# Optimization experiments

Measured on AMD Instinct MI355X. Metric: run time of the kernel, lower is better.

Reference implementation:

```python
import jax, jax.numpy as jnp
import numpy as np

ALPHA = 0.001
TAU = 1.0
KAPPA = 1.0
N_ITER = 1


def setup_inputs() -> dict:
    key = jax.random.key(0)
    k1, k2, k3, k4, k5 = jax.random.split(key, 5)
    B, H, N, K = 8, 8, 512, 16
    mu = jax.random.normal(k1, (B, N, K), dtype=jnp.float32)
    # beta: softmax-like attention weights over j (positive, rows sum to 1)
    beta = jax.nn.softmax(jax.random.normal(k2, (B, H, N, N), dtype=jnp.float32), axis=-1)
    mu_prior = jax.random.normal(k3, (B, N, K), dtype=jnp.float32)
    phi = 0.1 * jax.random.normal(k4, (B, N, 3), dtype=jnp.float32)
    g = jax.random.normal(k5, (3, K, K), dtype=jnp.float32)
    generators = 0.5 * (g - jnp.swapaxes(g, -1, -2))  # skew-symmetric so(3) rep -> stable expm
    lr = jnp.asarray(0.05, dtype=jnp.float32)
    return {"mu": mu, "beta": beta, "mu_prior": mu_prior, "phi": phi,
            "generators": generators, "lr": lr}


def _transport(mu, phi, generators):
    # phi_algebra[b,n] = sum_g phi[b,n,g] * G_g  -> (B,N,K,K)
    B, N, K = mu.shape
    phi_alg = jnp.einsum('bng,gkl->bnkl', phi, generators)
    expm = jax.vmap(jax.scipy.linalg.expm)
    Om_i = expm(phi_alg.reshape(B * N, K, K)).reshape(B, N, K, K)
    Om_j_inv = expm((-phi_alg).reshape(B * N, K, K)).reshape(B, N, K, K)
    # mu_t[b,i,j] = Om_i[b,i] @ (Om_j_inv[b,j] @ mu[b,j])  (factored, avoids (B,N,N,K,K))
    v = jnp.einsum('bjlm,bjm->bjl', Om_j_inv, mu)          # (B,N,K)
    mu_t = jnp.einsum('bikl,bjl->bijk', Om_i, v)           # (B,N,N,K)
    return mu_t


def reference(mu, beta, mu_prior, phi, generators, lr):
    beta_avg = beta.mean(axis=1)                           # (B,N,N)
    mu_cur = mu
    for _ in range(N_ITER):
        grad_prior = ALPHA * (mu_cur - mu_prior)
        mu_t = _transport(mu_cur, phi, generators)         # (B,N,N,K)
        delta = mu_cur[:, :, None, :] - mu_t               # (B,N,N,K)
        # TERM 1: sum_j (beta_ij/tau) * delta_ij
        grad1 = jnp.einsum('bij,bijk->bik', beta_avg, delta) / TAU
        # TERM 2 (second-order): sum_j sum_k (beta_ij/kappa)(delta_jk - beta_ik) KL_ij gkl_ik
        #   = (1/kappa)[ sum_j beta_ij KL_ij gkl_ij - (sum_j beta_ij KL_ij) * sum_k beta_ik gkl_ik ]
        kl = jnp.sum(delta * delta, axis=-1) / (2.0 * TAU)  # (B,N,N)
        gkl = delta / TAU                                   # (B,N,N,K)
        w = beta_avg * kl                                   # (B,N,N)
        term1 = jnp.einsum('bij,bijk->bik', w, gkl)
        s = jnp.sum(w, axis=-1)                             # (B,N)
        bsum = jnp.einsum('bij,bijk->bik', beta_avg, gkl)
        grad2 = (term1 - s[..., None] * bsum) / KAPPA
        mu_cur = mu_cur - lr * (grad_prior + grad1 + grad2)
    return mu_cur
```

## Files before the change

### kernel.cpp

```cpp
#include <hip/hip_runtime.h>
#include <hip/hip_bf16.h>
#include <cstddef>
#include <cstdint>

#define B_ 8
#define H_ 8
#define N_ 512
#define K_ 16
#define NN_ (N_*N_)

static constexpr float ALPHA_C = 0.001f;

typedef float f32x4 __attribute__((ext_vector_type(4)));

#define LDSTRIDE 20

__device__ __forceinline__ void mm_rowB(const float* a, const float* Bbuf,
                                        int c0, f32x4& acc)
{
    #pragma unroll
    for (int k = 0; k < 16; ++k) {
        const f32x4 bk = *(const f32x4*)&Bbuf[k * LDSTRIDE + c0];
        acc.x = fmaf(a[k], bk.x, acc.x);
        acc.y = fmaf(a[k], bk.y, acc.y);
        acc.z = fmaf(a[k], bk.z, acc.z);
        acc.w = fmaf(a[k], bk.w, acc.w);
    }
}

__device__ __forceinline__ void read_row(const float* buf, int r, float* a)
{
    #pragma unroll
    for (int i = 0; i < 4; ++i) {
        const f32x4 t = *(const f32x4*)&buf[r * LDSTRIDE + 4 * i];
        a[4*i]   = t.x; a[4*i+1] = t.y; a[4*i+2] = t.z; a[4*i+3] = t.w;
    }
}

__device__ __forceinline__ void write_strip(float* buf, int r, int c0, f32x4 s)
{
    *(f32x4*)&buf[r * LDSTRIDE + c0] = s;
}

__global__ __launch_bounds__(256) void expm_beta_kernel(
    const float* __restrict__ mu, const float* __restrict__ phi,
    const float* __restrict__ gen, const float* __restrict__ beta,
    float* __restrict__ Om, float* __restrict__ v, float* __restrict__ q,
    float* __restrict__ bavg)
{
    __shared__ float lds[4][2][16 * LDSTRIDE];

    const int tid  = threadIdx.x;
    const int w    = tid >> 6, lane = tid & 63;
    const int r    = lane >> 2, c0 = (lane & 3) << 2;
    const int bn   = (blockIdx.x << 2) | w;
    const int bb   = bn >> 9;
    const int nn   = bn & 511;

    float* U0 = lds[w][0];
    float* U1 = lds[w][1];

    const float p0 = phi[bn*3+0], p1 = phi[bn*3+1], p2 = phi[bn*3+2];
    const int gidx = r * 16 + c0;
    const f32x4 g0 = *(const f32x4*)&gen[gidx];
    const f32x4 g1 = *(const f32x4*)&gen[256 + gidx];
    const f32x4 g2 = *(const f32x4*)&gen[512 + gidx];
    const float mur = mu[bn * 16 + r];

    const size_t betaBase = (((size_t)bb * H_) * N_ + nn) * N_;
    const float* bp = beta + betaBase + (lane << 2);
    f32x4 bt[16];
    #pragma unroll
    for (int h = 0; h < H_; ++h) {
        bt[2*h+0] = __builtin_nontemporal_load((const f32x4*)(bp + (size_t)h * NN_));
        bt[2*h+1] = __builtin_nontemporal_load((const f32x4*)(bp + (size_t)h * NN_ + 256));
    }

    f32x4 As;
    As.x = p0*g0.x + p1*g1.x + p2*g2.x;
    As.y = p0*g0.y + p1*g1.y + p2*g2.y;
    As.z = p0*g0.z + p1*g1.z + p2*g2.z;
    As.w = p0*g0.w + p1*g1.w + p2*g2.w;

    float t = As.x*As.x + As.y*As.y + As.z*As.z + As.w*As.w;
    #pragma unroll
    for (int m = 1; m <= 32; m <<= 1) t += __shfl_xor(t, m, 64);
    float theta = sqrtf(t);
    int s = 0;
    while (theta > 2.0f && s < 30) { theta *= 0.5f; ++s; }
    const float sc = exp2f((float)(-s));
    const f32x4 Xs = As * sc;

    write_strip(U0, r, c0, Xs);
    float xrow[16];
    read_row(U0, r, xrow);

    {
        const f32x4 rv0 = (((bt[0]+bt[2]) + (bt[4]+bt[6]))
                         + ((bt[8]+bt[10]) + (bt[12]+bt[14]))) * 0.125f;
        const f32x4 rv1 = (((bt[1]+bt[3]) + (bt[5]+bt[7]))
                         + ((bt[9]+bt[11]) + (bt[13]+bt[15]))) * 0.125f;
        float* bo = bavg + (size_t)bn * N_ + (lane << 2);
        *(f32x4*)bo         = rv0;
        *(f32x4*)(bo + 256) = rv1;
    }

    f32x4 a2s = {0.f, 0.f, 0.f, 0.f};
    mm_rowB(xrow, U0, c0, a2s);
    write_strip(U1, r, c0, a2s);

    f32x4 a3s = {0.f, 0.f, 0.f, 0.f};
    mm_rowB(xrow, U1, c0, a3s);

    float a2row[16];
    read_row(U1, r, a2row);
    f32x4 a4s = {0.f, 0.f, 0.f, 0.f};
    mm_rowB(a2row, U1, c0, a4s);
    write_strip(U0, r, c0, a4s);
    float a4row[16];
    read_row(U0, r, a4row);

    f32x4 di = {0.f, 0.f, 0.f, 0.f};
    if (r >= c0 && r < c0 + 4) ((float*)&di)[r - c0] = 1.0f;

    const f32x4 C0 = di + Xs + a2s * 0.5f + a3s * (1.0f/6.0f);
    const f32x4 C1 = di * (1.0f/24.0f) + Xs * (1.0f/120.0f)
                   + a2s * (1.0f/720.0f) + a3s * (1.0f/5040.0f);
    const f32x4 Q2 = di * (1.0f/40320.0f) + Xs * (1.0f/362880.0f)
                   + a2s * (1.0f/3628800.0f) + a3s * (1.0f/39916800.0f)
                   + a4s * (1.0f/479001600.0f);

    write_strip(U1, r, c0, Q2);
    f32x4 T1 = C1;
    mm_rowB(a4row, U1, c0, T1);

    write_strip(U1, r, c0, T1);
    f32x4 P = C0;
    mm_rowB(a4row, U1, c0, P);

    for (int it = 0; it < s; ++it) {
        write_strip(U1, r, c0, P);
        float prow[16];
        read_row(U1, r, prow);
        f32x4 Pn = {0.f, 0.f, 0.f, 0.f};
        mm_rowB(prow, U1, c0, Pn);
        P = Pn;
    }

    *(f32x4*)&Om[(size_t)bn * 256 + r * 16 + c0] = P;

    f32x4 vc = P * mur;
    #pragma unroll
    for (int m = 4; m <= 32; m <<= 1) {
        vc.x += __shfl_xor(vc.x, m, 64);
        vc.y += __shfl_xor(vc.y, m, 64);
        vc.z += __shfl_xor(vc.z, m, 64);
        vc.w += __shfl_xor(vc.w, m, 64);
    }
    if (r == 0) *(f32x4*)&v[bn * 16 + c0] = vc;

    float qp = vc.x*vc.x + vc.y*vc.y + vc.z*vc.z + vc.w*vc.w;
    qp += __shfl_xor(qp, 1, 64);
    qp += __shfl_xor(qp, 2, 64);
    if (lane == 0) q[bn] = 0.5f * qp;
}

__device__ __forceinline__ float fold16(float* wc, int lane)
{
    #pragma unroll
    for (int k = 0; k < 8; ++k) {
        const bool up = (lane & 32) != 0;
        const float send = up ? wc[k] : wc[k + 8];
        const float recv = __shfl_xor(send, 32, 64);
        wc[k] = (up ? wc[k + 8] : wc[k]) + recv;
    }
    #pragma unroll
    for (int k = 0; k < 4; ++k) {
        const bool up = (lane & 16) != 0;
        const float send = up ? wc[k] : wc[k + 4];
        const float recv = __shfl_xor(send, 16, 64);
        wc[k] = (up ? wc[k + 4] : wc[k]) + recv;
    }
    #pragma unroll
    for (int k = 0; k < 2; ++k) {
        const bool up = (lane & 8) != 0;
        const float send = up ? wc[k] : wc[k + 2];
        const float recv = __shfl_xor(send, 8, 64);
        wc[k] = (up ? wc[k + 2] : wc[k]) + recv;
    }
    {
        const bool up = (lane & 4) != 0;
        const float send = up ? wc[0] : wc[1];
        const float recv = __shfl_xor(send, 4, 64);
        wc[0] = (up ? wc[1] : wc[0]) + recv;
    }
    wc[0] += __shfl_xor(wc[0], 2, 64);
    wc[0] += __shfl_xor(wc[0], 1, 64);
    return wc[0];
}

__device__ __forceinline__ float rot_reduce(const float* omr, float gv, int lane)
{
    float pr[4];
    #pragma unroll
    for (int rr = 0; rr < 4; ++rr) pr[rr] = omr[rr] * gv;

    #pragma unroll
    for (int k = 0; k < 2; ++k) {
        const bool up = (lane & 4) != 0;
        const float send = up ? pr[k] : pr[k + 2];
        const float recv = __shfl_xor(send, 4, 64);
        pr[k] = (up ? pr[k + 2] : pr[k]) + recv;
    }
    {
        const bool up = (lane & 8) != 0;
        const float send = up ? pr[0] : pr[1];
        const float recv = __shfl_xor(send, 8, 64);
        pr[0] = (up ? pr[1] : pr[0]) + recv;
    }
    pr[0] += __shfl_xor(pr[0], 16, 64);
    pr[0] += __shfl_xor(pr[0], 32, 64);
    return pr[0];
}

__global__ __launch_bounds__(256, 3) void grad_kernel(
    const float* __restrict__ mu, const float* __restrict__ mu_prior,
    const float* __restrict__ lrp, const float* __restrict__ Om,
    const float* __restrict__ v, const float* __restrict__ q,
    const float* __restrict__ bavg, float* __restrict__ out)
{
    __shared__ float v_t[16 * 516];
    __shared__ f32x4 q4[128];

    const int blk = blockIdx.x;
    const int b   = blk >> 7;
    const int i0  = (blk & 127) << 2;
    const int tid = threadIdx.x;
    const int wid = tid >> 6, lane = tid & 63;
    const int i   = i0 + wid;
    const size_t rowi = (size_t)b * N_ + i;

    const float* vb = v + (size_t)b * N_ * K_;
    f32x4 tq[8];
    #pragma unroll
    for (int s = 0; s < 8; ++s)
        tq[s] = *(const f32x4*)&vb[(tid + 256 * s) << 2];

    f32x4 qreg = {0.f, 0.f, 0.f, 0.f};
    const f32x4* qb4 = (const f32x4*)(q + (size_t)b * N_);
    if (tid < 128) qreg = qb4[tid];

    const float* bpr = bavg + rowi * N_ + (lane << 2);
    const f32x4 rv0 = *(const f32x4*)bpr;
    const f32x4 rv1 = *(const f32x4*)(bpr + 256);

    #pragma unroll
    for (int s = 0; s < 8; ++s) {
        const int f4 = tid + 256 * s;
        const int j  = f4 >> 2;
        const int k0 = (f4 & 3) << 2;
        v_t[(k0+0) * 516 + j] = tq[s].x;
        v_t[(k0+1) * 516 + j] = tq[s].y;
        v_t[(k0+2) * 516 + j] = tq[s].z;
        v_t[(k0+3) * 516 + j] = tq[s].w;
    }
    if (tid < 128) q4[tid] = qreg;
    __syncthreads();

    float vi[16];
    #pragma unroll
    for (int k = 0; k < 16; ++k) vi[k] = v_t[k * 516 + i];
    const float qi = ((const float*)q4)[i];

    const int j0 = lane << 2;

    float dA0 = 0.f, dA1 = 0.f, dA2 = 0.f, dA3 = 0.f;
    #pragma unroll
    for (int k = 0; k < 16; ++k) {
        const f32x4 vj = *(const f32x4*)&v_t[k * 516 + j0];
        dA0 = fmaf(vi[k], vj.x, dA0);
        dA1 = fmaf(vi[k], vj.y, dA1);
        dA2 = fmaf(vi[k], vj.z, dA2);
        dA3 = fmaf(vi[k], vj.w, dA3);
    }
    float dB0 = 0.f, dB1 = 0.f, dB2 = 0.f, dB3 = 0.f;
    #pragma unroll
    for (int k = 0; k < 16; ++k) {
        const f32x4 vj = *(const f32x4*)&v_t[k * 516 + j0 + 256];
        dB0 = fmaf(vi[k], vj.x, dB0);
        dB1 = fmaf(vi[k], vj.y, dB1);
        dB2 = fmaf(vi[k], vj.z, dB2);
        dB3 = fmaf(vi[k], vj.w, dB3);
    }

    const f32x4 qjA = q4[lane];
    const f32x4 qjB = q4[lane | 64];
    const float rklA0 = rv0.x * (qi + qjA.x - dA0);
    const float rklA1 = rv0.y * (qi + qjA.y - dA1);
    const float rklA2 = rv0.z * (qi + qjA.z - dA2);
    const float rklA3 = rv0.w * (qi + qjA.w - dA3);
    const float rklB0 = rv1.x * (qi + qjB.x - dB0);
    const float rklB1 = rv1.y * (qi + qjB.y - dB1);
    const float rklB2 = rv1.z * (qi + qjB.z - dB2);
    const float rklB3 = rv1.w * (qi + qjB.w - dB3);

    float sacc = ((rklA0 + rklA1) + (rklA2 + rklA3))
               + ((rklB0 + rklB1) + (rklB2 + rklB3));
    float R    = ((rv0.x + rv0.y) + (rv0.z + rv0.w))
               + ((rv1.x + rv1.y) + (rv1.z + rv1.w));

    const int cmine = (lane >> 2) & 15;
    const int tqi   = lane & 3;
    const float* omb = Om + rowi * 256;
    float omr[4];
    #pragma unroll
    for (int rr = 0; rr < 4; ++rr)
        omr[rr] = omb[(4 * tqi + rr) * 16 + cmine];

    const int row = 4 * tqi + 2 * ((lane >> 2) & 1) + ((lane >> 3) & 1);
    const size_t oi = rowi * 16 + row;
    float m0 = 0.f, mp = 0.f;
    if (lane < 16) { m0 = mu[oi]; mp = mu_prior[oi]; }
    const float lrv = lrp[0];

    #pragma unroll
    for (int off = 32; off > 0; off >>= 1) {
        sacc += __shfl_xor(sacc, off, 64);
        R    += __shfl_xor(R,    off, 64);
    }
    const float oms  = 1.0f - sacc;
    const float coef = oms * R + sacc;

    const float cA0 = fmaf(oms, rv0.x, rklA0);
    const float cA1 = fmaf(oms, rv0.y, rklA1);
    const float cA2 = fmaf(oms, rv0.z, rklA2);
    const float cA3 = fmaf(oms, rv0.w, rklA3);
    const float cB0 = fmaf(oms, rv1.x, rklB0);
    const float cB1 = fmaf(oms, rv1.y, rklB1);
    const float cB2 = fmaf(oms, rv1.z, rklB2);
    const float cB3 = fmaf(oms, rv1.w, rklB3);

    float wc[16];
    #pragma unroll
    for (int k = 0; k < 16; ++k) wc[k] = 0.f;

    #pragma unroll
    for (int k = 0; k < 16; ++k) {
        const f32x4 vj = *(const f32x4*)&v_t[k * 516 + j0];
        float t1 = fmaf(cA0, vj.x, wc[k]);
        t1 = fmaf(cA1, vj.y, t1);
        t1 = fmaf(cA2, vj.z, t1);
        wc[k] = fmaf(cA3, vj.w, t1);
    }
    #pragma unroll
    for (int k = 0; k < 16; ++k) {
        const f32x4 vj = *(const f32x4*)&v_t[k * 516 + j0 + 256];
        float t1 = fmaf(cB0, vj.x, wc[k]);
        t1 = fmaf(cB1, vj.y, t1);
        t1 = fmaf(cB2, vj.z, t1);
        wc[k] = fmaf(cB3, vj.w, t1);
    }

    const float wf = fold16(wc, lane);

    const float gv = coef * v_t[cmine * 516 + i] - wf;
    const float pr = rot_reduce(omr, gv, lane);

    if (lane < 16) {
        out[oi] = m0 - lrv * (ALPHA_C * (m0 - mp) + pr);
    }
}

extern "C" void kernel_launch(void* const* d_in, const int* in_sizes, int n_in,
                              void* d_out, int out_size, void* d_ws, size_t ws_size,
                              hipStream_t stream)
{
    const float* mu   = (const float*)d_in[0];
    const float* beta = (const float*)d_in[1];
    const float* mup  = (const float*)d_in[2];
    const float* phi  = (const float*)d_in[3];
    const float* gen  = (const float*)d_in[4];
    const float* lr   = (const float*)d_in[5];
    float* out = (float*)d_out;

    float* Om   = (float*)d_ws;
    float* v    = Om + (size_t)4096 * 256;
    float* q    = v  + (size_t)4096 * 16;
    float* bavg = q  + (size_t)4096;

    expm_beta_kernel<<<B_ * N_ / 4, 256, 0, stream>>>(mu, phi, gen, beta, Om, v, q, bavg);
    grad_kernel<<<B_ * (N_ / 4), 256, 0, stream>>>(mu, mup, lr, Om, v, q, bavg, out);
}
```

Baseline: 126.9 us.

## Move beta head-averaging from expm kernel into grad kernel

The head-mean of beta now happens inside the gradient kernel, which reads beta directly, instead of in the expm kernel. This removes the bavg intermediate buffer: an 8 MB write followed by a re-read. In exchange the grad kernel carries 16 extra vector registers of beta loads, and its launch bound of 3 blocks per SM is dropped, which may change occupancy. The expm kernel becomes light and no longer overlaps the beta streaming with its matrix-exponential math.

```diff
diff --git a/kernel.cpp b/kernel.cpp
--- a/kernel.cpp
+++ b/kernel.cpp
@@ -42,11 +42,10 @@
     *(f32x4*)&buf[r * LDSTRIDE + c0] = s;
 }
 
-__global__ __launch_bounds__(256) void expm_beta_kernel(
+__global__ __launch_bounds__(256) void expm_kernel(
     const float* __restrict__ mu, const float* __restrict__ phi,
-    const float* __restrict__ gen, const float* __restrict__ beta,
-    float* __restrict__ Om, float* __restrict__ v, float* __restrict__ q,
-    float* __restrict__ bavg)
+    const float* __restrict__ gen, float* __restrict__ Om,
+    float* __restrict__ v, float* __restrict__ q)
 {
     __shared__ float lds[4][2][16 * LDSTRIDE];
 
@@ -54,8 +53,6 @@
     const int w    = tid >> 6, lane = tid & 63;
     const int r    = lane >> 2, c0 = (lane & 3) << 2;
     const int bn   = (blockIdx.x << 2) | w;
-    const int bb   = bn >> 9;
-    const int nn   = bn & 511;
 
     float* U0 = lds[w][0];
     float* U1 = lds[w][1];
@@ -65,17 +62,6 @@
     const f32x4 g0 = *(const f32x4*)&gen[gidx];
     const f32x4 g1 = *(const f32x4*)&gen[256 + gidx];
     const f32x4 g2 = *(const f32x4*)&gen[512 + gidx];
-    const float mur = mu[bn * 16 + r];
-
-    const size_t betaBase = (((size_t)bb * H_) * N_ + nn) * N_;
-    const float* bp = beta + betaBase + (lane << 2);
-    f32x4 bt[16];
-    #pragma unroll
-    for (int h = 0; h < H_; ++h) {
-        bt[2*h+0] = __builtin_nontemporal_load((const f32x4*)(bp + (size_t)h * NN_));
-        bt[2*h+1] = __builtin_nontemporal_load((const f32x4*)(bp + (size_t)h * NN_ + 256));
-    }
-
     f32x4 As;
     As.x = p0*g0.x + p1*g1.x + p2*g2.x;
     As.y = p0*g0.y + p1*g1.y + p2*g2.y;
@@ -94,16 +80,6 @@
     write_strip(U0, r, c0, Xs);
     float xrow[16];
     read_row(U0, r, xrow);
-
-    {
-        const f32x4 rv0 = (((bt[0]+bt[2]) + (bt[4]+bt[6]))
-                         + ((bt[8]+bt[10]) + (bt[12]+bt[14]))) * 0.125f;
-        const f32x4 rv1 = (((bt[1]+bt[3]) + (bt[5]+bt[7]))
-                         + ((bt[9]+bt[11]) + (bt[13]+bt[15]))) * 0.125f;
-        float* bo = bavg + (size_t)bn * N_ + (lane << 2);
-        *(f32x4*)bo         = rv0;
-        *(f32x4*)(bo + 256) = rv1;
-    }
 
     f32x4 a2s = {0.f, 0.f, 0.f, 0.f};
     mm_rowB(xrow, U0, c0, a2s);
@@ -149,6 +125,7 @@
 
     *(f32x4*)&Om[(size_t)bn * 256 + r * 16 + c0] = P;
 
+    const float mur = mu[bn * 16 + r];
     f32x4 vc = P * mur;
     #pragma unroll
     for (int m = 4; m <= 32; m <<= 1) {
@@ -223,11 +200,11 @@
     return pr[0];
 }
 
-__global__ __launch_bounds__(256, 3) void grad_kernel(
-    const float* __restrict__ mu, const float* __restrict__ mu_prior,
-    const float* __restrict__ lrp, const float* __restrict__ Om,
-    const float* __restrict__ v, const float* __restrict__ q,
-    const float* __restrict__ bavg, float* __restrict__ out)
+__global__ void grad_kernel(
+    const float* __restrict__ mu, const float* __restrict__ beta,
+    const float* __restrict__ mu_prior, const float* __restrict__ lrp,
+    const float* __restrict__ Om, const float* __restrict__ v,
+    const float* __restrict__ q, float* __restrict__ out)
 {
     __shared__ float v_t[16 * 516];
     __shared__ f32x4 q4[128];
@@ -250,9 +227,13 @@
     const f32x4* qb4 = (const f32x4*)(q + (size_t)b * N_);
     if (tid < 128) qreg = qb4[tid];
 
-    const float* bpr = bavg + rowi * N_ + (lane << 2);
-    const f32x4 rv0 = *(const f32x4*)bpr;
-    const f32x4 rv1 = *(const f32x4*)(bpr + 256);
+    const float* bp = beta + (((size_t)b * H_) * N_ + i) * N_ + (lane << 2);
+    f32x4 bt[16];
+    #pragma unroll
+    for (int h = 0; h < H_; ++h) {
+        bt[2*h+0] = __builtin_nontemporal_load((const f32x4*)(bp + (size_t)h * NN_));
+        bt[2*h+1] = __builtin_nontemporal_load((const f32x4*)(bp + (size_t)h * NN_ + 256));
+    }
 
     #pragma unroll
     for (int s = 0; s < 8; ++s) {
@@ -266,6 +247,11 @@
     }
     if (tid < 128) q4[tid] = qreg;
     __syncthreads();
+
+    const f32x4 rv0 = (((bt[0]+bt[2]) + (bt[4]+bt[6]))
+                     + ((bt[8]+bt[10]) + (bt[12]+bt[14]))) * 0.125f;
+    const f32x4 rv1 = (((bt[1]+bt[3]) + (bt[5]+bt[7]))
+                     + ((bt[9]+bt[11]) + (bt[13]+bt[15]))) * 0.125f;
 
     float vi[16];
     #pragma unroll
@@ -383,11 +369,10 @@
     const float* lr   = (const float*)d_in[5];
     float* out = (float*)d_out;
 
-    float* Om   = (float*)d_ws;
-    float* v    = Om + (size_t)4096 * 256;
-    float* q    = v  + (size_t)4096 * 16;
-    float* bavg = q  + (size_t)4096;
-
-    expm_beta_kernel<<<B_ * N_ / 4, 256, 0, stream>>>(mu, phi, gen, beta, Om, v, q, bavg);
-    grad_kernel<<<B_ * (N_ / 4), 256, 0, stream>>>(mu, mup, lr, Om, v, q, bavg, out);
-}
+    float* Om = (float*)d_ws;
+    float* v  = Om + (size_t)4096 * 256;
+    float* q  = v  + (size_t)4096 * 16;
+
+    expm_kernel<<<B_ * N_ / 4, 256, 0, stream>>>(mu, phi, gen, Om, v, q);
+    grad_kernel<<<B_ * (N_ / 4), 256, 0, stream>>>(mu, beta, mup, lr, Om, v, q, out);
+}
```

New measurement: 168.0 us. 1.32x slower.
